# Kernel tuning notes

Measured on AMD Instinct MI355X. Metric: run time of the kernel, lower is better.

Reference implementation:

```python
import jax, jax.numpy as jnp
import numpy as np

SIGMA_DIS = 3.0  # from __init__ default sigma_dis=3
PRED_SCALE = 3e-6  # keep sqrt-norms below sigma so max(sigma - d, 0) is not saturated at 0


def setup_inputs() -> dict:
    key = jax.random.key(0)
    k1, k2 = jax.random.split(key)
    C, H, W = 8, 2048, 2048
    K = 32  # number of connected kernel components (labels 1..K, 0 = background)
    pred = jax.random.normal(k1, (C, H, W), dtype=jnp.float32) * PRED_SCALE
    kernel_labels = jax.random.randint(k2, (H, W), 0, K + 1, dtype=jnp.int32)
    regions_mask = jnp.ones((H, W), dtype=bool)  # unused by the original forward
    return {
        "pred_similarities": pred,
        "regions_mask": regions_mask,
        "kernel_labels": kernel_labels,
        "num_kernel": K,
    }


def _l_dis(pred, labels_flat, num_kernel, sigma):
    # pred: [C, H, W]; labels_flat: [H*W] int, values in 0..num_kernel (0 = background).
    C = pred.shape[0]
    flat = pred.reshape(C, -1).T  # [P, C]
    # Per-kernel, per-channel masked sums (the Gk broadcast values): S[k, c]
    S = jax.ops.segment_sum(flat, labels_flat, num_segments=num_kernel + 1)  # [K+1, C]
    # Per-kernel pixel counts N[k]
    N = jax.ops.segment_sum(jnp.ones_like(labels_flat, dtype=pred.dtype),
                            labels_flat, num_segments=num_kernel + 1)  # [K+1]
    # Gk_i has value S[i,c] on kernel i's pixels and 0 elsewhere; supports of distinct
    # kernels are disjoint, so ||Gk_i - Gk_j||_F^2 = N[i]*sum_c S[i,c]^2 + N[j]*sum_c S[j,c]^2.
    A = (N * jnp.sum(S * S, axis=1))[1:]  # [K], drop background label 0
    pair_sq = A[:, None] + A[None, :]  # [K, K]
    D = jnp.maximum(sigma - jnp.sqrt(pair_sq), 0.0)
    term = jnp.log(D * D + 1.0)
    upper = jnp.triu(jnp.ones((num_kernel, num_kernel), dtype=bool), k=1)  # i<j pairs
    L = jnp.sum(jnp.where(upper, term, 0.0))
    scale = (num_kernel - 1) / num_kernel  # 1.0/num_kernel * (num_kernel - 1)
    return L * jnp.asarray(scale, pred.dtype)


def reference(pred_similarities, regions_mask, kernel_labels, num_kernel):
    # regions_mask is accepted but unused, matching the original forward.
    labels_flat = kernel_labels.reshape(-1)
    return _l_dis(pred_similarities, labels_flat, num_kernel, SIGMA_DIS)
```

## Files before the change

### kernel.cpp

```cpp
#include <hip/hip_runtime.h>
#include <hip/hip_bf16.h>
#include <math.h>


typedef __attribute__((ext_vector_type(8))) short short8;
typedef __attribute__((ext_vector_type(4))) float f32x4;

constexpr int NSEGF = 32;
constexpr int RPS   = 9;
constexpr int NROWS = NSEGF * RPS;
constexpr int BLK   = 256;
constexpr int WPB   = 4;
constexpr int NBLK  = 1024;
constexpr int NWAVES= NBLK * WPB;
constexpr int TPX   = 128;
constexpr int STEPS = TPX / 32;
constexpr int L1BLK = 32;
constexpr int SLABS = NBLK / L1BLK;
constexpr int L1BASE   = 1024;
constexpr int PARTBASE = 16384;

#define SCHED_FENCE asm volatile("" ::: "memory")
#define WAITVM(n)   asm volatile("s_waitcnt vmcnt(" #n ")" ::: "memory")

typedef __attribute__((address_space(1))) void A1v;
typedef __attribute__((address_space(3))) void A3v;

__device__ __forceinline__ void gload16(const void* g, void* l) {
  __builtin_amdgcn_global_load_lds((const A1v*)g, (A3v*)l, 16, 0, 0);
}

__device__ __forceinline__ short f2bf(float f) {
  return (short)__bfloat16_as_ushort(__float2bfloat16(f));
}

__device__ __forceinline__ float wave_sum64(float x) {
  int t;
  t = __builtin_amdgcn_update_dpp(0, __float_as_int(x), 0x111, 0xf, 0xf, true); x += __int_as_float(t);
  t = __builtin_amdgcn_update_dpp(0, __float_as_int(x), 0x112, 0xf, 0xf, true); x += __int_as_float(t);
  t = __builtin_amdgcn_update_dpp(0, __float_as_int(x), 0x114, 0xf, 0xf, true); x += __int_as_float(t);
  t = __builtin_amdgcn_update_dpp(0, __float_as_int(x), 0x118, 0xf, 0xf, true); x += __int_as_float(t);
  t = __builtin_amdgcn_update_dpp(0, __float_as_int(x), 0x142, 0xf, 0xf, true); x += __int_as_float(t);
  t = __builtin_amdgcn_update_dpp(0, __float_as_int(x), 0x143, 0xf, 0xf, true); x += __int_as_float(t);
  return x;
}

__device__ __forceinline__ void stage_tile(const float* __restrict__ pred,
                                           const int*   __restrict__ lab,
                                           float* predbuf, int* labbuf,
                                           size_t px0, int lane, size_t P) {
#pragma unroll
  for (int i = 0; i < 4; ++i) {
    const int c   = 2 * i + (lane >> 5);
    const int swb = (((lane & 31) * 16) ^ ((c & 7) << 4));
    gload16(pred + (size_t)c * P + px0 + (swb >> 2), predbuf + i * 256);
  }
  if (lane < 32) gload16(lab + px0 + lane * 4, labbuf);
}

__device__ __forceinline__ void compute_tile(const float* __restrict__ pbuf,
                                             const int*   __restrict__ lbuf,
                                             int colq, int quad, int ms0, int ms1,
                                             short8 Bconst,
                                             f32x4& acc0, f32x4& acc1) {
  const short ONE = (short)0x3F80;
  const int  c    = colq & 7;
  const bool isch = (colq < 8);
  const char* prow = (const char*)(pbuf + c * TPX);
  const int*  lb   = lbuf + quad * 8;
#pragma unroll
  for (int s = 0; s < STEPS; ++s) {
    const int4 la = *(const int4*)(lb + s * 32);
    const int4 lc = *(const int4*)(lb + s * 32 + 4);
    const int  b0 = (s * 128 + quad * 32) ^ ((c & 7) << 4);
    const float4 x = *(const float4*)(prow + b0);
    const float4 y = *(const float4*)(prow + (b0 ^ 16));
    short8 A0, A1, B;
    A0[0] = (la.x == ms0) ? ONE : (short)0;
    A0[1] = (la.y == ms0) ? ONE : (short)0;
    A0[2] = (la.z == ms0) ? ONE : (short)0;
    A0[3] = (la.w == ms0) ? ONE : (short)0;
    A0[4] = (lc.x == ms0) ? ONE : (short)0;
    A0[5] = (lc.y == ms0) ? ONE : (short)0;
    A0[6] = (lc.z == ms0) ? ONE : (short)0;
    A0[7] = (lc.w == ms0) ? ONE : (short)0;
    A1[0] = (la.x == ms1) ? ONE : (short)0;
    A1[1] = (la.y == ms1) ? ONE : (short)0;
    A1[2] = (la.z == ms1) ? ONE : (short)0;
    A1[3] = (la.w == ms1) ? ONE : (short)0;
    A1[4] = (lc.x == ms1) ? ONE : (short)0;
    A1[5] = (lc.y == ms1) ? ONE : (short)0;
    A1[6] = (lc.z == ms1) ? ONE : (short)0;
    A1[7] = (lc.w == ms1) ? ONE : (short)0;
    if (isch) {
      B[0] = f2bf(x.x); B[1] = f2bf(x.y); B[2] = f2bf(x.z); B[3] = f2bf(x.w);
      B[4] = f2bf(y.x); B[5] = f2bf(y.y); B[6] = f2bf(y.z); B[7] = f2bf(y.w);
    } else {
      B = Bconst;
    }
    acc0 = __builtin_amdgcn_mfma_f32_16x16x32_bf16(A0, B, acc0, 0, 0, 0);
    acc1 = __builtin_amdgcn_mfma_f32_16x16x32_bf16(A1, B, acc1, 0, 0, 0);
  }
}

__global__ __launch_bounds__(BLK, 4)
void seg_mfma(const float* __restrict__ pred,
              const int*   __restrict__ lab,
              float*       __restrict__ ws,
              int P) {
  __shared__ __align__(16) float predL[WPB][2][8 * TPX];
  __shared__ __align__(16) int   labL[WPB][2][TPX];

  const int tid  = threadIdx.x;
  const int wid  = tid >> 6;
  const int lane = tid & 63;
  const int colq = lane & 15;
  const int quad = lane >> 4;
  const int ms0  = colq + 1;
  const int ms1  = colq + 17;

  const int bs = (blockIdx.x & 7) * (NBLK / 8) + (blockIdx.x >> 3);
  const int gw = bs * WPB + wid;

  const int spt = (P / TPX) / NWAVES;
  const size_t px00 = (size_t)gw * spt * TPX;

  f32x4 acc0 = {0.f, 0.f, 0.f, 0.f};
  f32x4 acc1 = {0.f, 0.f, 0.f, 0.f};

  short8 Bconst;
  {
    const short v = (colq == 8) ? (short)0x3F80 : (short)0;
#pragma unroll
    for (int i = 0; i < 8; ++i) Bconst[i] = v;
  }

  float* pb0 = &predL[wid][0][0];
  float* pb1 = &predL[wid][1][0];
  int*   lb0 = &labL[wid][0][0];
  int*   lb1 = &labL[wid][1][0];

  stage_tile(pred, lab, pb0, lb0, px00, lane, (size_t)P);
  stage_tile(pred, lab, pb1, lb1, px00 + TPX, lane, (size_t)P);

  for (int t = 0; t < spt; ++t) {
    if (t < spt - 1) { WAITVM(5); } else { WAITVM(0); }
    const float* pb = (t & 1) ? pb1 : pb0;
    const int*   lb = (t & 1) ? lb1 : lb0;
    compute_tile(pb, lb, colq, quad, ms0, ms1, Bconst, acc0, acc1);
    SCHED_FENCE;
    if (t + 2 < spt) {
      stage_tile(pred, lab, (t & 1) ? pb1 : pb0, (t & 1) ? lb1 : lb0,
                 px00 + (size_t)(t + 2) * TPX, lane, (size_t)P);
    }
  }

  float* redw = &predL[wid][0][0];
  SCHED_FENCE;
  if (colq < RPS) {
#pragma unroll
    for (int r = 0; r < 4; ++r)
      redw[(quad * 4 + r) * RPS + colq] = acc0[r];
#pragma unroll
    for (int r = 0; r < 4; ++r)
      redw[(16 + quad * 4 + r) * RPS + colq] = acc1[r];
  }
  __syncthreads();
  for (int v = tid; v < NROWS; v += BLK) {
    float s = 0.f;
#pragma unroll
    for (int w = 0; w < WPB; ++w) s += predL[w][0][v];
    ws[PARTBASE + (size_t)blockIdx.x * NROWS + v] = s;
  }
}

__global__ __launch_bounds__(256)
void reduce1(float* __restrict__ ws) {
  const int b = blockIdx.x;
  for (int v = threadIdx.x; v < NROWS; v += 256) {
    float s = 0.f;
#pragma unroll 4
    for (int i = 0; i < SLABS; ++i)
      s += ws[PARTBASE + (size_t)(b * SLABS + i) * NROWS + v];
    ws[L1BASE + (size_t)v * L1BLK + b] = s;
  }
}

__global__ __launch_bounds__(BLK)
void seg_gen(const float* __restrict__ pred,
             const int*   __restrict__ lab,
             float*       __restrict__ ws,
             int P, int C) {
  __shared__ float bins[(NSEGF + 1) * RPS];
  const int tid = threadIdx.x;
  for (int i = tid; i < (NSEGF + 1) * RPS; i += BLK) bins[i] = 0.f;
  __syncthreads();
  const int stride = gridDim.x * BLK;
  const int Cc = C < 8 ? C : 8;
  for (int p = blockIdx.x * BLK + tid; p < P; p += stride) {
    int lb = lab[p]; if (lb < 0) lb = 0; if (lb > NSEGF) lb = NSEGF;
    const int o = lb * RPS;
    unsafeAtomicAdd(&bins[o + 8], 1.f);
    for (int c = 0; c < Cc; ++c)
      unsafeAtomicAdd(&bins[o + c], pred[(size_t)c * P + p]);
  }
  __syncthreads();
  for (int i = tid; i < NROWS; i += BLK)
    ws[PARTBASE + (size_t)blockIdx.x * NROWS + i] = bins[RPS + i];
}

__global__ __launch_bounds__(256)
void finish_kernel(const float* __restrict__ ws,
                   const int*   __restrict__ nkp,
                   float*       __restrict__ out,
                   int C) {
  __shared__ float sfin[NROWS];
  __shared__ float sA[NSEGF + 1];
  __shared__ float wsum[4];
  int K = *nkp; if (K > NSEGF) K = NSEGF;
  const int tid = threadIdx.x;
  const int Cc = C < 8 ? C : 8;

  for (int v = tid; v < NROWS; v += 256) {
    const float* r = ws + L1BASE + (size_t)v * L1BLK;
    float s = 0.f;
#pragma unroll
    for (int b = 0; b < L1BLK; ++b) s += r[b];
    sfin[v] = s;
  }
  __syncthreads();
  for (int k = 1 + tid; k <= K; k += 256) {
    float s2 = 0.f;
    for (int c = 0; c < Cc; ++c) {
      const float v = sfin[(k - 1) * RPS + c];
      s2 = fmaf(v, v, s2);
    }
    sA[k] = sfin[(k - 1) * RPS + 8] * s2;
  }
  __syncthreads();

  const int npairs = K * (K - 1) / 2;
  float accv = 0.f;
  for (int idx = tid; idx < npairs; idx += 256) {
    int i = 1, rem = idx;
    while (rem >= K - i) { rem -= K - i; ++i; }
    const int j = i + 1 + rem;
    const float ps = sA[i] + sA[j];
    const float d  = fmaxf(3.0f - sqrtf(ps), 0.f);
    accv += logf(fmaf(d, d, 1.f));
  }
  accv = wave_sum64(accv);
  if ((tid & 63) == 63) wsum[tid >> 6] = accv;
  __syncthreads();
  if (tid == 0)
    out[0] = (wsum[0] + wsum[1] + wsum[2] + wsum[3]) * (float)(K - 1) / (float)K;
}

extern "C" void kernel_launch(void* const* d_in, const int* in_sizes, int n_in,
                              void* d_out, int out_size, void* d_ws, size_t ws_size,
                              hipStream_t stream) {
  const float* pred = (const float*)d_in[0];
  const int*   lab  = (const int*)d_in[2];
  const int*   nkp  = (const int*)d_in[3];
  float*       out  = (float*)d_out;
  float*       ws   = (float*)d_ws;

  const int P = in_sizes[2];
  const int C = in_sizes[0] / P;

  const size_t need = (size_t)(PARTBASE + (size_t)NBLK * NROWS) * sizeof(float);
  const int spt = (P / TPX) / NWAVES;
  const bool fast = (C == 8) && (P % (TPX * NWAVES)) == 0 && spt >= 2 &&
                    ws_size >= need;

  if (fast) {
    seg_mfma<<<NBLK, BLK, 0, stream>>>(pred, lab, ws, P);
  } else {
    seg_gen<<<NBLK, BLK, 0, stream>>>(pred, lab, ws, P, C);
  }
  reduce1<<<L1BLK, 256, 0, stream>>>(ws);
  finish_kernel<<<1, 256, 0, stream>>>(ws, nkp, out, C);
}
```

Before: 41.60 us.

## Triple-buffer LDS staging and halve block count in segment MFMA kernel

Moves the per-wave global-to-LDS pipeline from double to triple buffering, so two tiles stay in flight while one is computed, and adjusts the vmcnt waits to match. The grid shrinks from 1024 to 512 blocks, which doubles the tiles per wave, and the occupancy hint drops to 2 blocks per CU to make room for the larger shared memory footprint. The aim is to hide more memory latency in a bandwidth-bound reduction, at the cost of fewer resident waves and a longer serial loop per wave. The fast-path guard now needs at least 4 steps per wave.

```diff
diff --git a/kernel.cpp b/kernel.cpp
--- a/kernel.cpp
+++ b/kernel.cpp
@@ -11,10 +11,11 @@
 constexpr int NROWS = NSEGF * RPS;
 constexpr int BLK   = 256;
 constexpr int WPB   = 4;
-constexpr int NBLK  = 1024;
+constexpr int NBLK  = 512;
 constexpr int NWAVES= NBLK * WPB;
 constexpr int TPX   = 128;
 constexpr int STEPS = TPX / 32;
+constexpr int NBUF  = 3;
 constexpr int L1BLK = 32;
 constexpr int SLABS = NBLK / L1BLK;
 constexpr int L1BASE   = 1024;
@@ -103,13 +104,13 @@
   }
 }
 
-__global__ __launch_bounds__(BLK, 4)
+__global__ __launch_bounds__(BLK, 2)
 void seg_mfma(const float* __restrict__ pred,
               const int*   __restrict__ lab,
               float*       __restrict__ ws,
               int P) {
-  __shared__ __align__(16) float predL[WPB][2][8 * TPX];
-  __shared__ __align__(16) int   labL[WPB][2][TPX];
+  __shared__ __align__(16) float predL[WPB][NBUF][8 * TPX];
+  __shared__ __align__(16) int   labL[WPB][NBUF][TPX];
 
   const int tid  = threadIdx.x;
   const int wid  = tid >> 6;
@@ -135,24 +136,23 @@
     for (int i = 0; i < 8; ++i) Bconst[i] = v;
   }
 
-  float* pb0 = &predL[wid][0][0];
-  float* pb1 = &predL[wid][1][0];
-  int*   lb0 = &labL[wid][0][0];
-  int*   lb1 = &labL[wid][1][0];
-
-  stage_tile(pred, lab, pb0, lb0, px00, lane, (size_t)P);
-  stage_tile(pred, lab, pb1, lb1, px00 + TPX, lane, (size_t)P);
-
+  stage_tile(pred, lab, &predL[wid][0][0], &labL[wid][0][0], px00,            lane, (size_t)P);
+  stage_tile(pred, lab, &predL[wid][1][0], &labL[wid][1][0], px00 + TPX,      lane, (size_t)P);
+  stage_tile(pred, lab, &predL[wid][2][0], &labL[wid][2][0], px00 + 2 * TPX,  lane, (size_t)P);
+
+  int cur = 0;
   for (int t = 0; t < spt; ++t) {
-    if (t < spt - 1) { WAITVM(5); } else { WAITVM(0); }
-    const float* pb = (t & 1) ? pb1 : pb0;
-    const int*   lb = (t & 1) ? lb1 : lb0;
-    compute_tile(pb, lb, colq, quad, ms0, ms1, Bconst, acc0, acc1);
+    if (t < spt - 2)       { WAITVM(10); }
+    else if (t == spt - 2) { WAITVM(5); }
+    else                   { WAITVM(0); }
+    compute_tile(&predL[wid][cur][0], &labL[wid][cur][0],
+                 colq, quad, ms0, ms1, Bconst, acc0, acc1);
     SCHED_FENCE;
-    if (t + 2 < spt) {
-      stage_tile(pred, lab, (t & 1) ? pb1 : pb0, (t & 1) ? lb1 : lb0,
-                 px00 + (size_t)(t + 2) * TPX, lane, (size_t)P);
+    if (t + NBUF < spt) {
+      stage_tile(pred, lab, &predL[wid][cur][0], &labL[wid][cur][0],
+                 px00 + (size_t)(t + NBUF) * TPX, lane, (size_t)P);
     }
+    cur = (cur == NBUF - 1) ? 0 : cur + 1;
   }
 
   float* redw = &predL[wid][0][0];
@@ -270,7 +270,7 @@
 
   const size_t need = (size_t)(PARTBASE + (size_t)NBLK * NROWS) * sizeof(float);
   const int spt = (P / TPX) / NWAVES;
-  const bool fast = (C == 8) && (P % (TPX * NWAVES)) == 0 && spt >= 2 &&
+  const bool fast = (C == 8) && (P % (TPX * NWAVES)) == 0 && spt >= 4 &&
                     ws_size >= need;
 
   if (fast) {
```

New measurement: 43.40 us. 1.04x slower.

## Replace partial-sum reduce kernel with grouped global atomics

Applied to the files above, without the earlier changes.

Each block now atomically adds its per-row partial sums into one of 32 interleaved group slots in the workspace, instead of writing a full partial slab that a separate reduce1 kernel summed. A memset zeroes the small accumulation buffer up front, and the finish kernel sums the 32 group slots directly. This removes one kernel launch and the round trip through a large partial buffer, at the cost of a memset launch and contention from global float atomics.

```diff
diff --git a/kernel.cpp b/kernel.cpp
--- a/kernel.cpp
+++ b/kernel.cpp
@@ -14,11 +14,7 @@
 constexpr int NBLK  = 1024;
 constexpr int NWAVES= NBLK * WPB;
 constexpr int TPX   = 128;
-constexpr int STEPS = TPX / 32;
-constexpr int L1BLK = 32;
-constexpr int SLABS = NBLK / L1BLK;
-constexpr int L1BASE   = 1024;
-constexpr int PARTBASE = 16384;
+constexpr int NGRP  = 32;
 
 #define SCHED_FENCE asm volatile("" ::: "memory")
 #define WAITVM(n)   asm volatile("s_waitcnt vmcnt(" #n ")" ::: "memory")
@@ -69,7 +65,7 @@
   const char* prow = (const char*)(pbuf + c * TPX);
   const int*  lb   = lbuf + quad * 8;
 #pragma unroll
-  for (int s = 0; s < STEPS; ++s) {
+  for (int s = 0; s < 4; ++s) {
     const int4 la = *(const int4*)(lb + s * 32);
     const int4 lc = *(const int4*)(lb + s * 32 + 4);
     const int  b0 = (s * 128 + quad * 32) ^ ((c & 7) << 4);
@@ -166,23 +162,12 @@
       redw[(16 + quad * 4 + r) * RPS + colq] = acc1[r];
   }
   __syncthreads();
+  const int grp = blockIdx.x & (NGRP - 1);
   for (int v = tid; v < NROWS; v += BLK) {
     float s = 0.f;
 #pragma unroll
     for (int w = 0; w < WPB; ++w) s += predL[w][0][v];
-    ws[PARTBASE + (size_t)blockIdx.x * NROWS + v] = s;
-  }
-}
-
-__global__ __launch_bounds__(256)
-void reduce1(float* __restrict__ ws) {
-  const int b = blockIdx.x;
-  for (int v = threadIdx.x; v < NROWS; v += 256) {
-    float s = 0.f;
-#pragma unroll 4
-    for (int i = 0; i < SLABS; ++i)
-      s += ws[PARTBASE + (size_t)(b * SLABS + i) * NROWS + v];
-    ws[L1BASE + (size_t)v * L1BLK + b] = s;
+    unsafeAtomicAdd(&ws[v * NGRP + grp], s);
   }
 }
 
@@ -205,8 +190,11 @@
       unsafeAtomicAdd(&bins[o + c], pred[(size_t)c * P + p]);
   }
   __syncthreads();
-  for (int i = tid; i < NROWS; i += BLK)
-    ws[PARTBASE + (size_t)blockIdx.x * NROWS + i] = bins[RPS + i];
+  const int grp = blockIdx.x & (NGRP - 1);
+  for (int i = tid; i < NROWS; i += BLK) {
+    const float v = bins[RPS + i];
+    if (v != 0.f) unsafeAtomicAdd(&ws[i * NGRP + grp], v);
+  }
 }
 
 __global__ __launch_bounds__(256)
@@ -222,10 +210,10 @@
   const int Cc = C < 8 ? C : 8;
 
   for (int v = tid; v < NROWS; v += 256) {
-    const float* r = ws + L1BASE + (size_t)v * L1BLK;
+    const float* r = ws + (size_t)v * NGRP;
     float s = 0.f;
 #pragma unroll
-    for (int b = 0; b < L1BLK; ++b) s += r[b];
+    for (int b = 0; b < NGRP; ++b) s += r[b];
     sfin[v] = s;
   }
   __syncthreads();
@@ -268,7 +256,9 @@
   const int P = in_sizes[2];
   const int C = in_sizes[0] / P;
 
-  const size_t need = (size_t)(PARTBASE + (size_t)NBLK * NROWS) * sizeof(float);
+  hipMemsetAsync(d_ws, 0, (size_t)NROWS * NGRP * sizeof(float), stream);
+
+  const size_t need = (size_t)NROWS * NGRP * sizeof(float);
   const int spt = (P / TPX) / NWAVES;
   const bool fast = (C == 8) && (P % (TPX * NWAVES)) == 0 && spt >= 2 &&
                     ws_size >= need;
@@ -278,6 +268,5 @@
   } else {
     seg_gen<<<NBLK, BLK, 0, stream>>>(pred, lab, ws, P, C);
   }
-  reduce1<<<L1BLK, 256, 0, stream>>>(ws);
   finish_kernel<<<1, 256, 0, stream>>>(ws, nkp, out, C);
 }
```

After: 57.82 us. +39.0%, slower.
